# Performance work log

Measured on AMD Instinct MI355X. Metric: run time of the kernel, lower is better.

The kernel has to match this reference:

```python
import jax, jax.numpy as jnp
import numpy as np

N, E, G, H, C, DIN, DE = 20000, 320000, 32, 8, 56, 32, 5
HC = H * C  # 448
NEG_SLOPE = 0.2
EPS_BN = 1e-5


def _seg_softmax(scores, seg, num):
    # scores: [E, H], softmax over edges sharing the same target node
    m = jax.ops.segment_max(scores, seg, num_segments=num)
    e = jnp.exp(scores - m[seg])
    s = jax.ops.segment_sum(e, seg, num_segments=num)
    return e / (s[seg] + 1e-16)


def _add_self_loops(src, dst, eattr, n):
    # PyG fill_value='mean': self-loop edge_attr = mean of incoming edge_attr
    deg = jax.ops.segment_sum(jnp.ones((src.shape[0],), eattr.dtype), dst, num_segments=n)
    esum = jax.ops.segment_sum(eattr, dst, num_segments=n)
    loop_attr = esum / jnp.maximum(deg, 1.0)[:, None]
    ar = jnp.arange(n, dtype=src.dtype)
    return (jnp.concatenate([src, ar]), jnp.concatenate([dst, ar]),
            jnp.concatenate([eattr, loop_attr], axis=0))


def _gatv2(x, src, dst, eattr, Wl, Wr, We, att, bias, n):
    xl = (x @ Wl).reshape(n, H, C)  # source transform (messages)
    xr = (x @ Wr).reshape(n, H, C)  # target transform
    ee = (eattr @ We).reshape(-1, H, C)
    s = jax.nn.leaky_relu(xl[src] + xr[dst] + ee, NEG_SLOPE)  # [E, H, C]
    score = jnp.einsum('ehc,hc->eh', s, att)
    alpha = _seg_softmax(score, dst, n)
    out = jax.ops.segment_sum(alpha[..., None] * xl[src], dst, num_segments=n)
    return out.reshape(n, HC) + bias


def _bn(x, gamma, beta):
    m = x.mean(axis=0)
    v = x.var(axis=0)  # biased variance, as torch BatchNorm1d (training)
    return (x - m) * jax.lax.rsqrt(v + EPS_BN) * gamma + beta


def setup_inputs() -> dict:
    key = jax.random.key(0)
    ks = jax.random.split(key, 18)
    sc = lambda k, shape: (jax.random.normal(k, shape, jnp.float32) * 0.05)
    return {
        'x': jax.random.normal(ks[0], (N, DIN), jnp.float32),
        'edge_index': jax.random.randint(ks[1], (2, E), 0, N),
        'edge_attr': jax.random.normal(ks[2], (E, DE), jnp.float32),
        'batch': jnp.sort(jax.random.randint(ks[3], (N,), 0, G)),
        'Wl1': sc(ks[4], (DIN, HC)), 'Wr1': sc(ks[5], (DIN, HC)),
        'We1': sc(ks[6], (DE, HC)), 'att1': sc(ks[7], (H, C)),
        'bias1': jnp.zeros((HC,), jnp.float32),
        'Wl2': sc(ks[8], (HC, HC)), 'Wr2': sc(ks[9], (HC, HC)),
        'We2': sc(ks[10], (DE, HC)), 'att2': sc(ks[11], (H, C)),
        'bias2': jnp.zeros((HC,), jnp.float32),
        'bn_gamma': jnp.ones((HC,), jnp.float32),
        'bn_beta': jnp.zeros((HC,), jnp.float32),
        'Wlin': sc(ks[12], (HC, 18)),
        'blin': jnp.zeros((18,), jnp.float32),
    }


def reference(x, edge_index, edge_attr, batch, Wl1, Wr1, We1, att1, bias1,
              Wl2, Wr2, We2, att2, bias2, bn_gamma, bn_beta, Wlin, blin):
    src, dst = edge_index[0], edge_index[1]
    src2, dst2, ea2 = _add_self_loops(src, dst, edge_attr, N)
    # dropout is identity in eval
    h = _gatv2(x, src2, dst2, ea2, Wl1, Wr1, We1, att1, bias1, N)
    h = jax.nn.elu(h)
    h = _bn(h, bn_gamma, bn_beta)
    h = _gatv2(h, src2, dst2, ea2, Wl2, Wr2, We2, att2, bias2, N)
    # global mean pool per graph
    cnt = jax.ops.segment_sum(jnp.ones((N,), h.dtype), batch, num_segments=G)
    pooled = jax.ops.segment_sum(h, batch, num_segments=G) / jnp.maximum(cnt, 1.0)[:, None]
    pooled = _bn(pooled, bn_gamma, bn_beta)
    logits = pooled @ Wlin + blin
    return jax.nn.log_softmax(logits, axis=1)
```

## Files before the change

kernel.cpp:

```cpp
#include <hip/hip_runtime.h>
#include <hip/hip_bf16.h>

#define NN   20000
#define EE   320000
#define EN   340000
#define HH   8
#define CC   56
#define HC   448
#define DEA  5
#define EAS  8
#define DINN 32
#define GG   32
#define NEG  0.2f

#define SS   896
#define MT   157
#define NT   7

typedef short bf16x8 __attribute__((ext_vector_type(8)));
typedef float f32x4  __attribute__((ext_vector_type(4)));
typedef float f32x8  __attribute__((ext_vector_type(8)));

static __device__ __forceinline__ unsigned short f2bf(float f) {
  unsigned int u = __float_as_uint(f);
  u += 0x7fffu + ((u >> 16) & 1u);
  return (unsigned short)(u >> 16);
}

static __device__ __forceinline__ f32x8 bf8_to_f32x8(uint4 u) {
  f32x8 o;
  o[0] = __uint_as_float(u.x << 16); o[1] = __uint_as_float(u.x & 0xffff0000u);
  o[2] = __uint_as_float(u.y << 16); o[3] = __uint_as_float(u.y & 0xffff0000u);
  o[4] = __uint_as_float(u.z << 16); o[5] = __uint_as_float(u.z & 0xffff0000u);
  o[6] = __uint_as_float(u.w << 16); o[7] = __uint_as_float(u.w & 0xffff0000u);
  return o;
}

__global__ void k_deg(const int* __restrict__ dst, int* deg) {
  int e = blockIdx.x * 256 + threadIdx.x;
  if (e < EE) atomicAdd(&deg[dst[e]], 1);
}

__global__ __launch_bounds__(1024) void k_scan(const int* __restrict__ deg, int* offs,
                                               int* cursor) {
  __shared__ int tot[1024];
  int t = threadIdx.x;
  int base = t * 20;
  int loc[20];
  int s = 0;
  #pragma unroll
  for (int i = 0; i < 20; i++) {
    int idx = base + i;
    int v = (idx < NN) ? deg[idx] + 1 : 0;
    loc[i] = s;
    s += v;
  }
  tot[t] = s;
  __syncthreads();
  for (int o = 1; o < 1024; o <<= 1) {
    int v = (t >= o) ? tot[t - o] : 0;
    __syncthreads();
    tot[t] += v;
    __syncthreads();
  }
  int basesum = (t == 0) ? 0 : tot[t - 1];
  #pragma unroll
  for (int i = 0; i < 20; i++) {
    int idx = base + i;
    if (idx < NN) { offs[idx] = basesum + loc[i]; cursor[idx] = basesum + loc[i]; }
  }
  if (t == 1023) offs[NN] = tot[1023];
}

__global__ void k_scatter(const int* __restrict__ src, const int* __restrict__ dst,
                          const float* __restrict__ ea,
                          int* cursor, int* __restrict__ csr_src, float* __restrict__ csr_ea) {
  int i = blockIdx.x * 256 + threadIdx.x;
  if (i >= EE) return;
  int d = dst[i], s = src[i];
  float a[DEA];
  #pragma unroll
  for (int j = 0; j < DEA; j++) a[j] = ea[(size_t)i * DEA + j];
  int pos = atomicAdd(&cursor[d], 1);
  csr_src[pos] = s;
  float* o = csr_ea + (size_t)pos * EAS;
  #pragma unroll
  for (int j = 0; j < DEA; j++) o[j] = a[j];
}

#define XCN (NN * DINN)
#define W1N (SS * DINN)
#define W2N (SS * HC)
__global__ void k_aux(const int* __restrict__ offs,
                      int* __restrict__ csr_src, float* __restrict__ csr_ea,
                      const float* __restrict__ x, unsigned short* __restrict__ xb,
                      const float* __restrict__ Wl1, const float* __restrict__ Wr1,
                      unsigned short* __restrict__ W1t,
                      const float* __restrict__ Wl2, const float* __restrict__ Wr2,
                      unsigned short* __restrict__ W2t) {
  int i = blockIdx.x * 256 + threadIdx.x;
  if (i < NN) {
    int n = i;
    int e0 = offs[n], e1 = offs[n + 1] - 1;
    float a0 = 0.f, a1 = 0.f, a2 = 0.f, a3 = 0.f, a4 = 0.f;
    for (int e = e0; e < e1; e++) {
      const float* p = csr_ea + (size_t)e * EAS;
      a0 += p[0]; a1 += p[1]; a2 += p[2]; a3 += p[3]; a4 += p[4];
    }
    float inv = 1.f / fmaxf((float)(e1 - e0), 1.f);
    csr_src[e1] = n;
    float* o = csr_ea + (size_t)e1 * EAS;
    o[0] = a0 * inv; o[1] = a1 * inv; o[2] = a2 * inv; o[3] = a3 * inv; o[4] = a4 * inv;
    return;
  }
  i -= NN;
  if (i < XCN) { xb[i] = f2bf(x[i]); return; }
  i -= XCN;
  if (i < W1N) {
    int col = i / DINN, k = i - col * DINN;
    int cc = (col < HC) ? col : col - HC;
    const float* W = (col < HC) ? Wl1 : Wr1;
    W1t[i] = f2bf(W[(size_t)k * HC + cc]);
    return;
  }
  i -= W1N;
  if (i < W2N) {
    int col = i / HC, k = i - col * HC;
    int cc = (col < HC) ? col : col - HC;
    const float* W = (col < HC) ? Wl2 : Wr2;
    W2t[i] = f2bf(W[(size_t)k * HC + cc]);
  }
}

__global__ __launch_bounds__(256) void k_gemm1(const unsigned short* __restrict__ xb,
                                               const unsigned short* __restrict__ W1t,
                                               unsigned short* __restrict__ out) {
  int w = threadIdx.x >> 6, lane = threadIdx.x & 63;
  int q = lane >> 4, r = lane & 15;
  int m0 = (blockIdx.x * 4 + w) * 16;
  int n0 = blockIdx.y * 64;
  int arow = m0 + r; if (arow >= NN) arow = NN - 1;
  bf16x8 a = *(const bf16x8*)(xb + (size_t)arow * DINN + q * 8);
  #pragma unroll
  for (int j = 0; j < 4; j++) {
    bf16x8 b = *(const bf16x8*)(W1t + (size_t)(n0 + j * 16 + r) * DINN + q * 8);
    f32x4 acc = {0.f, 0.f, 0.f, 0.f};
    acc = __builtin_amdgcn_mfma_f32_16x16x32_bf16(a, b, acc, 0, 0, 0);
    int col = n0 + j * 16 + r;
    #pragma unroll
    for (int reg = 0; reg < 4; reg++) {
      int row = m0 + q * 4 + reg;
      if (row < NN) out[(size_t)row * SS + col] = f2bf(acc[reg]);
    }
  }
}

__global__ __launch_bounds__(256) void k_attn(
    const unsigned short* __restrict__ xlr,
    const int* __restrict__ offs, const int* __restrict__ csr_src,
    const float* __restrict__ csr_ea,
    const float* __restrict__ We, const float* __restrict__ att,
    const float* __restrict__ bias,
    unsigned short* __restrict__ outb, float* __restrict__ outf, int layer1) {
  int n = blockIdx.x * 4 + (threadIdx.x >> 6);
  if (n >= NN) return;
  int lane = threadIdx.x & 63;
  int head = lane >> 3, sub = lane & 7;
  bool v = sub < 7;
  int cb = head * 56 + (v ? sub : 6) * 8;

  f32x8 z = {0.f,0.f,0.f,0.f,0.f,0.f,0.f,0.f};
  f32x8 xr = bf8_to_f32x8(*(const uint4*)(xlr + (size_t)n * SS + HC + cb));
  f32x8 at = *(const f32x8*)(att + cb);
  if (!v) at = z;
  f32x8 w0 = *(const f32x8*)(We + 0 * HC + cb);
  f32x8 w1 = *(const f32x8*)(We + 1 * HC + cb);
  f32x8 w2 = *(const f32x8*)(We + 2 * HC + cb);
  f32x8 w3 = *(const f32x8*)(We + 3 * HC + cb);
  f32x8 w4 = *(const f32x8*)(We + 4 * HC + cb);

  int e0 = offs[n], e1 = offs[n + 1];
  float l = 0.f;
  f32x8 acc = z;

  for (int e = e0; e < e1; e += 2) {
    int eb = e + 1;
    bool h2v = eb < e1;
    int ebc = h2v ? eb : e;
    int s0 = csr_src[e];
    int s1 = csr_src[ebc];
    const float* ep0 = csr_ea + (size_t)e * EAS;
    const float* ep1 = csr_ea + (size_t)ebc * EAS;
    f32x4 ea0 = *(const f32x4*)ep0;  float e40 = ep0[4];
    f32x4 ea1 = *(const f32x4*)ep1;  float e41 = ep1[4];
    uint4 g0 = *(const uint4*)(xlr + (size_t)s0 * SS + cb);
    uint4 g1 = *(const uint4*)(xlr + (size_t)s1 * SS + cb);
    f32x8 xl0 = bf8_to_f32x8(g0);
    f32x8 xl1 = bf8_to_f32x8(g1);

    f32x8 t0 = xl0 + xr;
    t0 += ea0.x * w0; t0 += ea0.y * w1; t0 += ea0.z * w2; t0 += ea0.w * w3; t0 += e40 * w4;
    f32x8 t1 = xl1 + xr;
    t1 += ea1.x * w0; t1 += ea1.y * w1; t1 += ea1.z * w2; t1 += ea1.w * w3; t1 += e41 * w4;
    #pragma unroll
    for (int i = 0; i < 8; i++) {
      t0[i] = fmaxf(t0[i], NEG * t0[i]);
      t1[i] = fmaxf(t1[i], NEG * t1[i]);
    }
    float p0 = 0.f, p1 = 0.f;
    #pragma unroll
    for (int i = 0; i < 8; i++) { p0 += t0[i] * at[i]; p1 += t1[i] * at[i]; }
    p0 += __shfl_xor(p0, 1, 64);  p1 += __shfl_xor(p1, 1, 64);
    p0 += __shfl_xor(p0, 2, 64);  p1 += __shfl_xor(p1, 2, 64);
    p0 += __shfl_xor(p0, 4, 64);  p1 += __shfl_xor(p1, 4, 64);
    float wv0 = __expf(fminf(p0, 60.f));
    float wv1 = h2v ? __expf(fminf(p1, 60.f)) : 0.f;
    acc += wv0 * xl0;
    acc += wv1 * xl1;
    l += wv0 + wv1;
  }

  f32x8 b8 = *(const f32x8*)(bias + cb);
  f32x8 o = acc * (1.f / (l + 1e-16f)) + b8;
  if (layer1) {
    if (v) {
      #pragma unroll
      for (int i = 0; i < 8; i++) o[i] = o[i] > 0.f ? o[i] : (__expf(o[i]) - 1.f);
      uint4 pk;
      pk.x = ((unsigned int)f2bf(o[1]) << 16) | f2bf(o[0]);
      pk.y = ((unsigned int)f2bf(o[3]) << 16) | f2bf(o[2]);
      pk.z = ((unsigned int)f2bf(o[5]) << 16) | f2bf(o[4]);
      pk.w = ((unsigned int)f2bf(o[7]) << 16) | f2bf(o[6]);
      *(uint4*)(outb + (size_t)n * HC + cb) = pk;
    }
  } else if (v) {
    float* dst = outf + (size_t)n * HC + cb;
    *(f32x4*)dst       = (f32x4){o[0], o[1], o[2], o[3]};
    *(f32x4*)(dst + 4) = (f32x4){o[4], o[5], o[6], o[7]};
  }
}

__global__ __launch_bounds__(448) void k_bnstats(const unsigned short* __restrict__ h,
                                                 float* stat) {
  int c = threadIdx.x;
  int rows_per = (NN + gridDim.x - 1) / gridDim.x;
  int r0 = blockIdx.x * rows_per, r1 = min(NN, r0 + rows_per);
  float s = 0.f, sq = 0.f;
  for (int r = r0; r < r1; r++) {
    unsigned int u = h[(size_t)r * HC + c];
    float v = __uint_as_float(u << 16);
    s += v; sq += v * v;
  }
  atomicAdd(&stat[c], s);
  atomicAdd(&stat[HC + c], sq);
}

__global__ __launch_bounds__(64) void k_w2fix(const unsigned short* __restrict__ W2t,
                                              const float* __restrict__ stat,
                                              const float* __restrict__ gam,
                                              const float* __restrict__ bet,
                                              unsigned short* __restrict__ W2s,
                                              float* __restrict__ bias2) {
  int j = blockIdx.x;
  int t = threadIdx.x;
  float bacc = 0.f;
  #pragma unroll
  for (int it = 0; it < 7; it++) {
    int k = t + it * 64;
    float w = __uint_as_float((unsigned int)W2t[(size_t)j * HC + k] << 16);
    float mean = stat[k] * (1.f / NN);
    float var  = stat[HC + k] * (1.f / NN) - mean * mean;
    float sc = rsqrtf(var + 1e-5f) * gam[k];
    float sh = bet[k] - mean * sc;
    bacc += sh * w;
    W2s[(size_t)j * HC + k] = f2bf(sc * w);
  }
  #pragma unroll
  for (int m = 32; m >= 1; m >>= 1) bacc += __shfl_xor(bacc, m, 64);
  if (t == 0) bias2[j] = bacc;
}

__global__ __launch_bounds__(256) void k_gemm2(const unsigned short* __restrict__ A,
                                               const unsigned short* __restrict__ Bt,
                                               const float* __restrict__ bias2,
                                               unsigned short* __restrict__ out) {
  __shared__ unsigned short As[128 * 64];
  __shared__ unsigned short Bs[128 * 64];
  int bid = blockIdx.x;
  int g = bid / 56, rem = bid - g * 56;
  int xs = min(8, MT - g * 8);
  int bx = g * 8 + rem % xs;
  int by = rem / xs;
  int t = threadIdx.x;
  int w = t >> 6, lane = t & 63;
  int wm = w >> 1, wn = w & 1;
  int q = lane >> 4, r = lane & 15;
  int m0 = bx * 128;
  int n0 = by * 128;

  const unsigned short *ag[4], *bg[4];
  unsigned short *la[4], *lb[4];
  #pragma unroll
  for (int j = 0; j < 4; j++) {
    int s = t + j * 256;
    int row = s >> 3, part = s & 7;
    int ar = m0 + row; if (ar >= NN) ar = NN - 1;
    ag[j] = A + (size_t)ar * HC + part * 8;
    bg[j] = Bt + (size_t)(n0 + row) * HC + part * 8;
    la[j] = As + s * 8;
    lb[j] = Bs + s * 8;
  }

  f32x4 zero = {0.f, 0.f, 0.f, 0.f};
  f32x4 acc[4][4];
  #pragma unroll
  for (int i = 0; i < 4; i++)
    #pragma unroll
    for (int j = 0; j < 4; j++) acc[i][j] = zero;

  for (int k0 = 0; k0 < HC; k0 += 64) {
    #pragma unroll
    for (int j = 0; j < 4; j++) {
      __builtin_amdgcn_global_load_lds(
          (const __attribute__((address_space(1))) unsigned int*)(ag[j] + k0),
          (__attribute__((address_space(3))) unsigned int*)la[j], 16, 0, 0);
      __builtin_amdgcn_global_load_lds(
          (const __attribute__((address_space(1))) unsigned int*)(bg[j] + k0),
          (__attribute__((address_space(3))) unsigned int*)lb[j], 16, 0, 0);
    }
    __syncthreads();
    #pragma unroll
    for (int kk = 0; kk < 64; kk += 32) {
      bf16x8 af[4], bf[4];
      #pragma unroll
      for (int i = 0; i < 4; i++)
        af[i] = *(const bf16x8*)(As + (wm * 64 + i * 16 + r) * 64 + kk + q * 8);
      #pragma unroll
      for (int j = 0; j < 4; j++)
        bf[j] = *(const bf16x8*)(Bs + (wn * 64 + j * 16 + r) * 64 + kk + q * 8);
      #pragma unroll
      for (int i = 0; i < 4; i++)
        #pragma unroll
        for (int j = 0; j < 4; j++)
          acc[i][j] = __builtin_amdgcn_mfma_f32_16x16x32_bf16(af[i], bf[j], acc[i][j], 0, 0, 0);
    }
    __syncthreads();
  }

  #pragma unroll
  for (int j = 0; j < 4; j++) {
    int col = n0 + wn * 64 + j * 16 + r;
    float bs = bias2[col];
    #pragma unroll
    for (int i = 0; i < 4; i++) {
      int row_base = m0 + wm * 64 + i * 16 + q * 4;
      #pragma unroll
      for (int reg = 0; reg < 4; reg++) {
        int row = row_base + reg;
        if (row < NN) out[(size_t)row * SS + col] = f2bf(acc[i][j][reg] + bs);
      }
    }
  }
}

__global__ __launch_bounds__(448) void k_pool(const float* __restrict__ h2,
                                              const int* __restrict__ batch,
                                              float* pooled, int* cnt) {
  int c = threadIdx.x;
  int rows_per = (NN + gridDim.x - 1) / gridDim.x;
  int r0 = blockIdx.x * rows_per, r1 = min(NN, r0 + rows_per);
  if (r0 >= r1) return;
  float loc = 0.f;
  int rc = 0;
  int gcur = batch[r0];
  for (int r = r0; r < r1; r++) {
    int g = batch[r];
    if (g != gcur) {
      atomicAdd(&pooled[gcur * HC + c], loc);
      if (c == 0) atomicAdd(&cnt[gcur], rc);
      loc = 0.f; rc = 0; gcur = g;
    }
    loc += h2[(size_t)r * HC + c];
    rc++;
  }
  atomicAdd(&pooled[gcur * HC + c], loc);
  if (c == 0) atomicAdd(&cnt[gcur], rc);
}

__global__ __launch_bounds__(448) void k_final(const float* __restrict__ pooled_sum,
                                               const int* __restrict__ cnt,
                                               const float* __restrict__ gam,
                                               const float* __restrict__ bet,
                                               const float* __restrict__ Wlin,
                                               const float* __restrict__ blin,
                                               float* __restrict__ out) {
  __shared__ float P[GG * HC];
  __shared__ float L[GG * 18];
  __shared__ float red[GG];
  int c = threadIdx.x;
  float s = 0.f, sq = 0.f;
  for (int g = 0; g < GG; g++) {
    float v = pooled_sum[g * HC + c] / fmaxf((float)cnt[g], 1.f);
    P[g * HC + c] = v; s += v; sq += v * v;
  }
  float mean = s * (1.f / GG);
  float var  = sq * (1.f / GG) - mean * mean;
  float sc = rsqrtf(var + 1e-5f) * gam[c];
  float sh = bet[c] - mean * sc;
  for (int g = 0; g < GG; g++) P[g * HC + c] = P[g * HC + c] * sc + sh;
  __syncthreads();
  for (int o = c; o < GG * 18; o += HC) {
    int g = o / 18, j = o - g * 18;
    float acc = blin[j];
    for (int k = 0; k < HC; k++) acc += P[g * HC + k] * Wlin[k * 18 + j];
    L[o] = acc;
  }
  __syncthreads();
  if (c < GG) {
    float mx = -3.4e38f;
    for (int j = 0; j < 18; j++) mx = fmaxf(mx, L[c * 18 + j]);
    float se = 0.f;
    for (int j = 0; j < 18; j++) se += __expf(L[c * 18 + j] - mx);
    red[c] = mx + logf(se);
  }
  __syncthreads();
  for (int o = c; o < GG * 18; o += HC) out[o] = L[o] - red[o / 18];
}

extern "C" void kernel_launch(void* const* d_in, const int* in_sizes, int n_in,
                              void* d_out, int out_size, void* d_ws, size_t ws_size,
                              hipStream_t stream) {
  (void)in_sizes; (void)n_in; (void)out_size; (void)ws_size;
  const float* x     = (const float*)d_in[0];
  const int*   ei    = (const int*)d_in[1];
  const float* ea    = (const float*)d_in[2];
  const int*   batch = (const int*)d_in[3];
  const float* Wl1   = (const float*)d_in[4];
  const float* Wr1   = (const float*)d_in[5];
  const float* We1   = (const float*)d_in[6];
  const float* att1  = (const float*)d_in[7];
  const float* bias1 = (const float*)d_in[8];
  const float* Wl2   = (const float*)d_in[9];
  const float* Wr2   = (const float*)d_in[10];
  const float* We2   = (const float*)d_in[11];
  const float* att2  = (const float*)d_in[12];
  const float* bias2in = (const float*)d_in[13];
  const float* gam   = (const float*)d_in[14];
  const float* bet   = (const float*)d_in[15];
  const float* Wlin  = (const float*)d_in[16];
  const float* blin  = (const float*)d_in[17];
  float* out = (float*)d_out;
  const int* srcp = ei;
  const int* dstp = ei + EE;

  char* ws = (char*)d_ws;
  size_t off = 0;
  auto alloc = [&](size_t bytes) -> char* {
    char* p = ws + off;
    off = (off + bytes + 255) & ~(size_t)255;
    return p;
  };
  int*   deg     = (int*)  alloc(NN * 4);
  float* bnstat  = (float*)alloc(HC * 2 * 4);
  float* pooled  = (float*)alloc(GG * HC * 4 + GG * 4);
  int*   cnt     = (int*)(pooled + GG * HC);
  size_t zlen    = (size_t)((char*)(cnt + GG) - (char*)deg);

  int*   offs    = (int*)  alloc((NN + 1) * 4);
  int*   cursor  = (int*)  alloc(NN * 4);
  int*   csr_src = (int*)  alloc((size_t)EN * 4);
  float* csr_ea  = (float*)alloc((size_t)EN * EAS * 4);
  unsigned short* xlr = (unsigned short*)alloc((size_t)NN * SS * 2);
  unsigned short* h1b = (unsigned short*)alloc((size_t)NN * HC * 2);
  float* h1f     = (float*)alloc((size_t)NN * HC * 4);
  unsigned short* xb  = (unsigned short*)alloc((size_t)NN * DINN * 2);
  unsigned short* W1t = (unsigned short*)alloc((size_t)SS * DINN * 2);
  unsigned short* W2t = (unsigned short*)alloc((size_t)SS * HC * 2);
  unsigned short* W2s = (unsigned short*)alloc((size_t)SS * HC * 2);
  float* bias2   = (float*)alloc(SS * 4);

  hipMemsetAsync(deg, 0, zlen, stream);
  k_deg<<<(EE + 255) / 256, 256, 0, stream>>>(dstp, deg);
  k_scan<<<1, 1024, 0, stream>>>(deg, offs, cursor);
  k_scatter<<<(EE + 255) / 256, 256, 0, stream>>>(srcp, dstp, ea, cursor, csr_src, csr_ea);
  k_aux<<<(NN + XCN + W1N + W2N + 255) / 256, 256, 0, stream>>>(
      offs, csr_src, csr_ea, x, xb, Wl1, Wr1, W1t, Wl2, Wr2, W2t);

  dim3 g1((NN + 63) / 64, SS / 64);
  k_gemm1<<<g1, 256, 0, stream>>>(xb, W1t, xlr);
  k_attn<<<(NN + 3) / 4, 256, 0, stream>>>(xlr, offs, csr_src, csr_ea,
                                           We1, att1, bias1, h1b, h1f, 1);
  k_bnstats<<<256, HC, 0, stream>>>(h1b, bnstat);
  k_w2fix<<<SS, 64, 0, stream>>>(W2t, bnstat, gam, bet, W2s, bias2);

  k_gemm2<<<MT * NT, 256, 0, stream>>>(h1b, W2s, bias2, xlr);
  k_attn<<<(NN + 3) / 4, 256, 0, stream>>>(xlr, offs, csr_src, csr_ea,
                                           We2, att2, bias2in, h1b, h1f, 0);

  k_pool<<<640, HC, 0, stream>>>(h1f, batch, pooled, cnt);
  k_final<<<1, HC, 0, stream>>>(pooled, cnt, gam, bet, Wlin, blin, out);
}
```

Baseline: 461.4 us.

## Split each node's edges across two waves, swizzle GEMM LDS, vectorize CSR stores

The attention kernel now gives each target node two wavefronts. Each wave processes alternating edge pairs, and the partial accumulators are merged through shared memory. This doubles the memory-level parallelism for the gather-heavy edge loop, at the cost of a block-wide sync and an LDS merge. The layer-2 GEMM gets an XOR swizzle on the LDS tile layout to cut bank conflicts. The CSR edge-attribute writes become two 16-byte vector stores, with zero padding.

```diff
diff --git a/kernel.cpp b/kernel.cpp
--- a/kernel.cpp
+++ b/kernel.cpp
@@ -84,8 +84,8 @@
   int pos = atomicAdd(&cursor[d], 1);
   csr_src[pos] = s;
   float* o = csr_ea + (size_t)pos * EAS;
-  #pragma unroll
-  for (int j = 0; j < DEA; j++) o[j] = a[j];
+  *(f32x4*)o       = (f32x4){a[0], a[1], a[2], a[3]};
+  *(f32x4*)(o + 4) = (f32x4){a[4], 0.f, 0.f, 0.f};
 }
 
 #define XCN (NN * DINN)
@@ -110,7 +110,8 @@
     float inv = 1.f / fmaxf((float)(e1 - e0), 1.f);
     csr_src[e1] = n;
     float* o = csr_ea + (size_t)e1 * EAS;
-    o[0] = a0 * inv; o[1] = a1 * inv; o[2] = a2 * inv; o[3] = a3 * inv; o[4] = a4 * inv;
+    *(f32x4*)o       = (f32x4){a0 * inv, a1 * inv, a2 * inv, a3 * inv};
+    *(f32x4*)(o + 4) = (f32x4){a4 * inv, 0.f, 0.f, 0.f};
     return;
   }
   i -= NN;
@@ -162,8 +163,12 @@
     const float* __restrict__ We, const float* __restrict__ att,
     const float* __restrict__ bias,
     unsigned short* __restrict__ outb, float* __restrict__ outf, int layer1) {
-  int n = blockIdx.x * 4 + (threadIdx.x >> 6);
-  if (n >= NN) return;
+  __shared__ float accL[2][64][8];
+  __shared__ float lL[2][64];
+  int wid  = threadIdx.x >> 6;
+  int slot = wid >> 1;
+  int half = wid & 1;
+  int n = blockIdx.x * 2 + slot;
   int lane = threadIdx.x & 63;
   int head = lane >> 3, sub = lane & 7;
   bool v = sub < 7;
@@ -183,7 +188,7 @@
   float l = 0.f;
   f32x8 acc = z;
 
-  for (int e = e0; e < e1; e += 2) {
+  for (int e = e0 + 2 * half; e < e1; e += 4) {
     int eb = e + 1;
     bool h2v = eb < e1;
     int ebc = h2v ? eb : e;
@@ -219,6 +224,19 @@
     acc += wv1 * xl1;
     l += wv0 + wv1;
   }
+
+  if (half == 1) {
+    *(f32x4*)&accL[slot][lane][0] = (f32x4){acc[0], acc[1], acc[2], acc[3]};
+    *(f32x4*)&accL[slot][lane][4] = (f32x4){acc[4], acc[5], acc[6], acc[7]};
+    lL[slot][lane] = l;
+  }
+  __syncthreads();
+  if (half == 1) return;
+  f32x4 alo = *(f32x4*)&accL[slot][lane][0];
+  f32x4 ahi = *(f32x4*)&accL[slot][lane][4];
+  acc[0] += alo.x; acc[1] += alo.y; acc[2] += alo.z; acc[3] += alo.w;
+  acc[4] += ahi.x; acc[5] += ahi.y; acc[6] += ahi.z; acc[7] += ahi.w;
+  l += lL[slot][lane];
 
   f32x8 b8 = *(const f32x8*)(bias + cb);
   f32x8 o = acc * (1.f / (l + 1e-16f)) + b8;
@@ -303,10 +321,11 @@
   #pragma unroll
   for (int j = 0; j < 4; j++) {
     int s = t + j * 256;
-    int row = s >> 3, part = s & 7;
+    int row = s >> 3;
+    int gcol = (s & 7) ^ (row & 7);
     int ar = m0 + row; if (ar >= NN) ar = NN - 1;
-    ag[j] = A + (size_t)ar * HC + part * 8;
-    bg[j] = Bt + (size_t)(n0 + row) * HC + part * 8;
+    ag[j] = A + (size_t)ar * HC + gcol * 8;
+    bg[j] = Bt + (size_t)(n0 + row) * HC + gcol * 8;
     la[j] = As + s * 8;
     lb[j] = Bs + s * 8;
   }
@@ -331,13 +350,18 @@
     __syncthreads();
     #pragma unroll
     for (int kk = 0; kk < 64; kk += 32) {
+      int p = (kk >> 3) + q;
       bf16x8 af[4], bf[4];
       #pragma unroll
-      for (int i = 0; i < 4; i++)
-        af[i] = *(const bf16x8*)(As + (wm * 64 + i * 16 + r) * 64 + kk + q * 8);
+      for (int i = 0; i < 4; i++) {
+        int row = wm * 64 + i * 16 + r;
+        af[i] = *(const bf16x8*)(As + row * 64 + ((p ^ (r & 7)) * 8));
+      }
       #pragma unroll
-      for (int j = 0; j < 4; j++)
-        bf[j] = *(const bf16x8*)(Bs + (wn * 64 + j * 16 + r) * 64 + kk + q * 8);
+      for (int j = 0; j < 4; j++) {
+        int row = wn * 64 + j * 16 + r;
+        bf[j] = *(const bf16x8*)(Bs + row * 64 + ((p ^ (r & 7)) * 8));
+      }
       #pragma unroll
       for (int i = 0; i < 4; i++)
         #pragma unroll
@@ -488,14 +512,14 @@
 
   dim3 g1((NN + 63) / 64, SS / 64);
   k_gemm1<<<g1, 256, 0, stream>>>(xb, W1t, xlr);
-  k_attn<<<(NN + 3) / 4, 256, 0, stream>>>(xlr, offs, csr_src, csr_ea,
-                                           We1, att1, bias1, h1b, h1f, 1);
+  k_attn<<<NN / 2, 256, 0, stream>>>(xlr, offs, csr_src, csr_ea,
+                                     We1, att1, bias1, h1b, h1f, 1);
   k_bnstats<<<256, HC, 0, stream>>>(h1b, bnstat);
   k_w2fix<<<SS, 64, 0, stream>>>(W2t, bnstat, gam, bet, W2s, bias2);
 
   k_gemm2<<<MT * NT, 256, 0, stream>>>(h1b, W2s, bias2, xlr);
-  k_attn<<<(NN + 3) / 4, 256, 0, stream>>>(xlr, offs, csr_src, csr_ea,
-                                           We2, att2, bias2in, h1b, h1f, 0);
+  k_attn<<<NN / 2, 256, 0, stream>>>(xlr, offs, csr_src, csr_ea,
+                                     We2, att2, bias2in, h1b, h1f, 0);
 
   k_pool<<<640, HC, 0, stream>>>(h1f, batch, pooled, cnt);
   k_final<<<1, HC, 0, stream>>>(pooled, cnt, gam, bet, Wlin, blin, out);
```

New measurement: 465.0 us. About the same (+0.8%).
